# Performance work log

Measured on AMD Instinct MI355X. Metric: run time of the kernel, lower is better.

## Reference

```python
import jax, jax.numpy as jnp
import numpy as np

B, S, D = 2, 2048, 4096
NH, NKV, HD = 32, 8, 128
NREP = NH // NKV
ROPE_THETA = 10000.0


def setup_inputs() -> dict:
    key = jax.random.key(0)
    k1, k2, k3, k4, k5 = jax.random.split(key, 5)
    x = jax.random.normal(k1, (B, S, D), jnp.float32)
    wq = jax.random.normal(k2, (NH * HD, D), jnp.float32) * 0.02
    wk = jax.random.normal(k3, (NKV * HD, D), jnp.float32) * 0.02
    wv = jax.random.normal(k4, (NKV * HD, D), jnp.float32) * 0.02
    wo = jax.random.normal(k5, (D, NH * HD), jnp.float32) * 0.02
    inv_freq = 1.0 / (ROPE_THETA ** (np.arange(0, HD, 2, dtype=np.float64) / HD))
    ang = np.outer(np.arange(S, dtype=np.float64), inv_freq)  # [S, HD/2]
    return {
        'x': x, 'start_pos': 0,
        'freqs_cos': jnp.asarray(np.cos(ang), jnp.float32),
        'freqs_sin': jnp.asarray(np.sin(ang), jnp.float32),
        'wq': wq, 'wk': wk, 'wv': wv, 'wo': wo,
    }


def _apply_rope(x, cos, sin):
    # x: [B, S, H, HD]; cos/sin: [S, HD/2]. Matches torch view_as_complex on
    # interleaved (even, odd) feature pairs: (xr + i*xi) * (cos + i*sin).
    xr = x[..., 0::2]
    xi = x[..., 1::2]
    c = cos[None, :, None, :]
    s = sin[None, :, None, :]
    out_r = xr * c - xi * s
    out_i = xr * s + xi * c
    return jnp.stack([out_r, out_i], axis=-1).reshape(x.shape)


def reference(x, start_pos, freqs_cos, freqs_sin, wq, wk, wv, wo):
    b, s, _ = x.shape
    xq = (x @ wq.T).reshape(b, s, NH, HD)
    xk = (x @ wk.T).reshape(b, s, NKV, HD)
    xv = (x @ wv.T).reshape(b, s, NKV, HD)
    # Source applies RoPE to K and V (not Q) -- reproduced faithfully.
    xk = _apply_rope(xk, freqs_cos, freqs_sin)
    xv = _apply_rope(xv, freqs_cos, freqs_sin)
    # start_pos == 0 prefill: cache slice [:, :start_pos+s] == freshly written xk/xv.
    # repeat_kv: head h_out = h_kv * NREP + rep  ==  jnp.repeat along head axis.
    keys = jnp.repeat(xk, NREP, axis=2)    # [B, S, NH, HD]
    values = jnp.repeat(xv, NREP, axis=2)  # [B, S, NH, HD]
    scale = 1.0 / jnp.sqrt(jnp.asarray(HD, x.dtype))
    scores = jnp.einsum('bqhd,bkhd->bhqk', xq, keys) * scale  # [B, NH, S, S]
    probs = jax.nn.softmax(scores, axis=-1)  # NOTE: no causal mask in source
    out = jnp.einsum('bhqk,bkhd->bqhd', probs, values).reshape(b, s, NH * HD)
    return out @ wo.T
```

## Files before the change

### kernel.cpp

```cpp
#include <hip/hip_runtime.h>
#include <hip/hip_bf16.h>


typedef short bf16x8 __attribute__((ext_vector_type(8)));
typedef float f32x4 __attribute__((ext_vector_type(4)));

__device__ __forceinline__ void load16(const void* g, void* l) {
  __builtin_amdgcn_global_load_lds(
      (const __attribute__((address_space(1))) void*)g,
      (__attribute__((address_space(3))) void*)l, 16, 0, 0);
}

__device__ __forceinline__ f32x4 mfma16(bf16x8 a, bf16x8 b, f32x4 c) {
  return __builtin_amdgcn_mfma_f32_16x16x32_bf16(a, b, c, 0, 0, 0);
}

__device__ __forceinline__ unsigned short f2b(float f) {
  union { float f; unsigned int u; } v; v.f = f;
  unsigned int u = v.u;
  return (unsigned short)((u + 0x7fffu + ((u >> 16) & 1u)) >> 16);
}
__device__ __forceinline__ float b2f(unsigned short u) {
  union { unsigned int u; float f; } v; v.u = ((unsigned int)u) << 16;
  return v.f;
}
__device__ __forceinline__ unsigned short f2b_fast(float f) {
  __hip_bfloat16 h = __float2bfloat16(f);
  return *reinterpret_cast<unsigned short*>(&h);
}

#define QSCALE (0.08838834764831845f * 1.4426950408889634f)

__global__ __launch_bounds__(256) void cvt_f32_bf16(
    const float* __restrict__ in, unsigned short* __restrict__ out, int n4) {
  int idx = blockIdx.x * 256 + threadIdx.x;
  int stride = gridDim.x * 256;
  for (int i = idx; i < n4; i += stride) {
    float4 v = reinterpret_cast<const float4*>(in)[i];
    ushort4 o;
    o.x = f2b(v.x); o.y = f2b(v.y); o.z = f2b(v.z); o.w = f2b(v.w);
    reinterpret_cast<ushort4*>(out)[i] = o;
  }
}

template <typename OutT>
__global__ __launch_bounds__(512, 2) void gemm256(
    const unsigned short* __restrict__ A, const unsigned short* __restrict__ Bw,
    OutT* __restrict__ C, int M, int N, int K, int sbl) {
  extern __shared__ char smem[];
  const int tid = threadIdx.x;
  const int lane = tid & 63;
  const int w = tid >> 6;
  const int lr = lane & 15, lg = lane >> 4;
  const int wr = w >> 2, wc = w & 3;

  const int nbn = N >> 8;
  const int bid = blockIdx.x, nwg = gridDim.x;
  const int swz = (bid & 7) * (nwg >> 3) + (bid >> 3);
  const int bm = swz / nbn, bn = swz % nbn;

  const unsigned short* Ag = A + (size_t)bm * 256 * K;
  const unsigned short* Bg = Bw + (size_t)bn * 256 * K;

  int aoffs[4], boffs[4], sdst[4];
#pragma unroll
  for (int j = 0; j < 4; ++j) {
    const int c = tid + j * 512;
    const int u = c >> 3;
    const int slot = ((c & 7) ^ (u & 7)) << 3;
    aoffs[j] = u * K + slot;
    const int br = ((u & 127) >> 5) * 64 + (u >> 7) * 32 + (u & 31);
    boffs[j] = br * K + slot;
    sdst[j] = ((tid & ~63) << 4) + j * 8192;
  }

#define ST_A(hh, tt)                                                          \
  {                                                                           \
    char* d = smem + (((tt)&1) * 65536);                                      \
    load16(Ag + aoffs[(hh)] + ((tt) << 6), d + sdst[(hh)]);                   \
    load16(Ag + aoffs[(hh) + 2] + ((tt) << 6), d + sdst[(hh) + 2]);           \
  }
#define ST_B(hh, tt)                                                          \
  {                                                                           \
    char* d = smem + (((tt)&1) * 65536) + 32768;                              \
    load16(Bg + boffs[(hh)*2] + ((tt) << 6), d + sdst[(hh)*2]);               \
    load16(Bg + boffs[(hh)*2 + 1] + ((tt) << 6), d + sdst[(hh)*2 + 1]);       \
  }
#define GATE10                                                                \
  asm volatile("s_waitcnt vmcnt(10)" ::: "memory");                           \
  __builtin_amdgcn_s_barrier();
#define LGKM0                                                                 \
  asm volatile("s_waitcnt lgkmcnt(0)" ::: "memory");                          \
  __builtin_amdgcn_sched_barrier(0);

  f32x4 acc[8][4];
#pragma unroll
  for (int m = 0; m < 8; ++m)
#pragma unroll
    for (int n = 0; n < 4; ++n) acc[m][n] = (f32x4){0.f, 0.f, 0.f, 0.f};

  ST_A(0, 0); ST_B(0, 0); ST_B(1, 0); ST_A(1, 0);
  ST_A(0, 1); ST_B(0, 1); ST_B(1, 1);

  const int NT = K >> 6;
  const int NI = NT >> 1;
  const int xr = (lr & 7) << 4;
  const int aBase = (wr * 128 + lr) * 128;
  const int bBase = (wc * 32 + lr) * 128;
  const int col0 = (lg * 16) ^ xr;
  const int col1 = (64 + lg * 16) ^ xr;

  bf16x8 aR[4][2], b01[2][2], b23[2][2];

  for (int i = 0; i < NI; ++i) {
    const int T1 = 2 * i + 1;
    const int te = (2 * i + 2 < NT) ? 2 * i + 2 : 0;
    const int to = (2 * i + 3 < NT) ? 2 * i + 3 : 1;
    const char* d0 = smem;
    const char* d1 = smem + 65536;

    GATE10;
#pragma unroll
    for (int mf = 0; mf < 4; ++mf) {
      aR[mf][0] = *(const bf16x8*)(d0 + aBase + mf * 2048 + col0);
      aR[mf][1] = *(const bf16x8*)(d0 + aBase + mf * 2048 + col1);
    }
#pragma unroll
    for (int nf = 0; nf < 2; ++nf) {
      b01[nf][0] = *(const bf16x8*)(d0 + 32768 + bBase + nf * 2048 + col0);
      b01[nf][1] = *(const bf16x8*)(d0 + 32768 + bBase + nf * 2048 + col1);
    }
    ST_A(1, T1);
    LGKM0;
    __builtin_amdgcn_s_setprio(1);
#pragma unroll
    for (int mf = 0; mf < 4; ++mf)
#pragma unroll
      for (int nf = 0; nf < 2; ++nf) {
        acc[mf][nf] = mfma16(aR[mf][0], b01[nf][0], acc[mf][nf]);
        acc[mf][nf] = mfma16(aR[mf][1], b01[nf][1], acc[mf][nf]);
      }
    __builtin_amdgcn_s_setprio(0);

    GATE10;
#pragma unroll
    for (int nf = 0; nf < 2; ++nf) {
      b23[nf][0] = *(const bf16x8*)(d0 + 32768 + 16384 + bBase + nf * 2048 + col0);
      b23[nf][1] = *(const bf16x8*)(d0 + 32768 + 16384 + bBase + nf * 2048 + col1);
    }
    ST_A(0, te);
    LGKM0;
    __builtin_amdgcn_s_setprio(1);
#pragma unroll
    for (int mf = 0; mf < 4; ++mf)
#pragma unroll
      for (int nf = 0; nf < 2; ++nf) {
        acc[mf][2 + nf] = mfma16(aR[mf][0], b23[nf][0], acc[mf][2 + nf]);
        acc[mf][2 + nf] = mfma16(aR[mf][1], b23[nf][1], acc[mf][2 + nf]);
      }
    __builtin_amdgcn_s_setprio(0);

    GATE10;
#pragma unroll
    for (int mf = 0; mf < 4; ++mf) {
      aR[mf][0] = *(const bf16x8*)(d0 + aBase + (4 + mf) * 2048 + col0);
      aR[mf][1] = *(const bf16x8*)(d0 + aBase + (4 + mf) * 2048 + col1);
    }
    ST_B(0, te);
    LGKM0;
    __builtin_amdgcn_s_setprio(1);
#pragma unroll
    for (int mf = 0; mf < 4; ++mf)
#pragma unroll
      for (int nf = 0; nf < 2; ++nf) {
        acc[4 + mf][nf] = mfma16(aR[mf][0], b01[nf][0], acc[4 + mf][nf]);
        acc[4 + mf][nf] = mfma16(aR[mf][1], b01[nf][1], acc[4 + mf][nf]);
      }
    __builtin_amdgcn_s_setprio(0);

    ST_B(1, te);
    __builtin_amdgcn_s_setprio(1);
#pragma unroll
    for (int mf = 0; mf < 4; ++mf)
#pragma unroll
      for (int nf = 0; nf < 2; ++nf) {
        acc[4 + mf][2 + nf] = mfma16(aR[mf][0], b23[nf][0], acc[4 + mf][2 + nf]);
        acc[4 + mf][2 + nf] = mfma16(aR[mf][1], b23[nf][1], acc[4 + mf][2 + nf]);
      }
    __builtin_amdgcn_s_setprio(0);

    GATE10;
#pragma unroll
    for (int mf = 0; mf < 4; ++mf) {
      aR[mf][0] = *(const bf16x8*)(d1 + aBase + mf * 2048 + col0);
      aR[mf][1] = *(const bf16x8*)(d1 + aBase + mf * 2048 + col1);
    }
#pragma unroll
    for (int nf = 0; nf < 2; ++nf) {
      b01[nf][0] = *(const bf16x8*)(d1 + 32768 + bBase + nf * 2048 + col0);
      b01[nf][1] = *(const bf16x8*)(d1 + 32768 + bBase + nf * 2048 + col1);
    }
    ST_A(1, te);
    LGKM0;
    __builtin_amdgcn_s_setprio(1);
#pragma unroll
    for (int mf = 0; mf < 4; ++mf)
#pragma unroll
      for (int nf = 0; nf < 2; ++nf) {
        acc[mf][nf] = mfma16(aR[mf][0], b01[nf][0], acc[mf][nf]);
        acc[mf][nf] = mfma16(aR[mf][1], b01[nf][1], acc[mf][nf]);
      }
    __builtin_amdgcn_s_setprio(0);

    GATE10;
#pragma unroll
    for (int nf = 0; nf < 2; ++nf) {
      b23[nf][0] = *(const bf16x8*)(d1 + 32768 + 16384 + bBase + nf * 2048 + col0);
      b23[nf][1] = *(const bf16x8*)(d1 + 32768 + 16384 + bBase + nf * 2048 + col1);
    }
    ST_A(0, to);
    LGKM0;
    __builtin_amdgcn_s_setprio(1);
#pragma unroll
    for (int mf = 0; mf < 4; ++mf)
#pragma unroll
      for (int nf = 0; nf < 2; ++nf) {
        acc[mf][2 + nf] = mfma16(aR[mf][0], b23[nf][0], acc[mf][2 + nf]);
        acc[mf][2 + nf] = mfma16(aR[mf][1], b23[nf][1], acc[mf][2 + nf]);
      }
    __builtin_amdgcn_s_setprio(0);

    GATE10;
#pragma unroll
    for (int mf = 0; mf < 4; ++mf) {
      aR[mf][0] = *(const bf16x8*)(d1 + aBase + (4 + mf) * 2048 + col0);
      aR[mf][1] = *(const bf16x8*)(d1 + aBase + (4 + mf) * 2048 + col1);
    }
    ST_B(0, to);
    LGKM0;
    __builtin_amdgcn_s_setprio(1);
#pragma unroll
    for (int mf = 0; mf < 4; ++mf)
#pragma unroll
      for (int nf = 0; nf < 2; ++nf) {
        acc[4 + mf][nf] = mfma16(aR[mf][0], b01[nf][0], acc[4 + mf][nf]);
        acc[4 + mf][nf] = mfma16(aR[mf][1], b01[nf][1], acc[4 + mf][nf]);
      }
    __builtin_amdgcn_s_setprio(0);

    ST_B(1, to);
    __builtin_amdgcn_s_setprio(1);
#pragma unroll
    for (int mf = 0; mf < 4; ++mf)
#pragma unroll
      for (int nf = 0; nf < 2; ++nf) {
        acc[4 + mf][2 + nf] = mfma16(aR[mf][0], b23[nf][0], acc[4 + mf][2 + nf]);
        acc[4 + mf][2 + nf] = mfma16(aR[mf][1], b23[nf][1], acc[4 + mf][2 + nf]);
      }
    __builtin_amdgcn_s_setprio(0);
  }
#undef ST_A
#undef ST_B
#undef GATE10
#undef LGKM0

  const float cscale = (bn < sbl) ? QSCALE : 1.0f;
#pragma unroll
  for (int mf = 0; mf < 8; ++mf)
#pragma unroll
    for (int nf = 0; nf < 4; ++nf)
#pragma unroll
      for (int r = 0; r < 4; ++r) {
        int rowc = bm * 256 + wr * 128 + mf * 16 + lg * 4 + r;
        int colc = bn * 256 + wc * 64 + nf * 16 + lr;
        float v = acc[mf][nf][r] * cscale;
        if constexpr (sizeof(OutT) == 2)
          C[(size_t)rowc * N + colc] = (OutT)f2b(v);
        else
          C[(size_t)rowc * N + colc] = v;
      }
}

__global__ __launch_bounds__(256) void rope_kv(
    const unsigned short* __restrict__ XQKV,
    const float* __restrict__ fc, const float* __restrict__ fs,
    unsigned short* __restrict__ Kr, unsigned short* __restrict__ Vt) {
  __shared__ unsigned short Vl[128][66];
  const int t = threadIdx.x;
  const int bid = blockIdx.x;
  const int stile = bid & 31, bkv = bid >> 5;
  const int b = bkv >> 3, kvh = bkv & 7;
  const int s0 = stile * 64;
  const int l = t & 63;
  const int jrow = t >> 6;

  for (int j = 0; j < 16; ++j) {
    int s = s0 + j * 4 + jrow;
    ushort2 v = *(const ushort2*)(XQKV + (size_t)(b * 2048 + s) * 6144 + 4096 +
                                  kvh * 128 + 2 * l);
    float c = fc[s * 64 + l], sn = fs[s * 64 + l];
    float xr = b2f(v.x), xi = b2f(v.y);
    ushort2 o;
    o.x = f2b(xr * c - xi * sn);
    o.y = f2b(xr * sn + xi * c);
    *(ushort2*)(Kr + ((size_t)bkv * 2048 + s) * 128 + 2 * l) = o;
  }
  for (int j = 0; j < 16; ++j) {
    int ss = j * 4 + jrow;
    int s = s0 + ss;
    ushort2 v = *(const ushort2*)(XQKV + (size_t)(b * 2048 + s) * 6144 + 5120 +
                                  kvh * 128 + 2 * l);
    float c = fc[s * 64 + l], sn = fs[s * 64 + l];
    float xr = b2f(v.x), xi = b2f(v.y);
    Vl[2 * l][ss] = f2b(xr * c - xi * sn);
    Vl[2 * l + 1][ss] = f2b(xr * sn + xi * c);
  }
  __syncthreads();
  const int d = t >> 1, half = t & 1;
  unsigned short* vdst = Vt + ((size_t)bkv * 128 + d) * 2048 + s0 + half * 32;
#pragma unroll
  for (int e = 0; e < 32; e += 4) {
    ushort4 pk;
    pk.x = Vl[d][half * 32 + e];
    pk.y = Vl[d][half * 32 + e + 1];
    pk.z = Vl[d][half * 32 + e + 2];
    pk.w = Vl[d][half * 32 + e + 3];
    *(ushort4*)(vdst + e) = pk;
  }
}

__global__ __launch_bounds__(256, 2) void attn_fwd(
    const unsigned short* __restrict__ XQ, const unsigned short* __restrict__ Kr,
    const unsigned short* __restrict__ Vt, unsigned short* __restrict__ AO) {
  extern __shared__ char smem[];
  char* Ksm = smem;
  char* Vsm = smem + 16384;
  unsigned short* Ps = (unsigned short*)(smem + 32768);
  const int t = threadIdx.x;
  const int lane = t & 63, w = t >> 6;
  const int lr = lane & 15, lg = lane >> 4;

  const int bid = blockIdx.x;
  const int nwg = gridDim.x;
  const int swz = (bid & 7) * (nwg >> 3) + (bid >> 3);
  const int qt = swz & 7;
  const int bh = swz >> 3;
  const int b = bh >> 5, h = bh & 31;
  const int bkv = b * 8 + (h >> 2);

  bf16x8 qf[4][4];
#pragma unroll
  for (int q4 = 0; q4 < 4; ++q4) {
    const unsigned short* qp =
        XQ + ((size_t)(b * 2048 + qt * 256 + w * 64 + q4 * 16 + lr)) * 6144 +
        h * 128 + lg * 8;
#pragma unroll
    for (int dc = 0; dc < 4; ++dc) qf[q4][dc] = *(const bf16x8*)(qp + dc * 32);
  }

  f32x4 acc[4][8];
#pragma unroll
  for (int q4 = 0; q4 < 4; ++q4)
#pragma unroll
    for (int i = 0; i < 8; ++i) acc[q4][i] = (f32x4){0.f, 0.f, 0.f, 0.f};
  float l_[4][4];
#pragma unroll
  for (int q4 = 0; q4 < 4; ++q4)
#pragma unroll
    for (int r = 0; r < 4; ++r) l_[q4][r] = 0.f;

  const unsigned short* Kbase = Kr + (size_t)bkv * 2048 * 128;
  const unsigned short* Vbase = Vt + (size_t)bkv * 128 * 2048;

  const int c0 = t, c1 = t + 256;
  const int kK0 = c0 & 31, dC0 = c0 >> 5;
  const int kK1 = c1 & 31, dC1 = c1 >> 5;
  const int vD0 = c0 & 127, vKc0 = c0 >> 7;
  const int vD1 = c1 & 127, vKc1 = c1 >> 7;
  const int dstb0 = (c0 & ~63) * 16;
  const int dstb1 = (c1 & ~63) * 16;

#define STAGE_KV(bufi, kt)                                                     \
  {                                                                            \
    char* kd = Ksm + (bufi)*8192;                                              \
    char* vd = Vsm + (bufi)*8192;                                              \
    load16(Kbase + (size_t)((kt)*32 + kK0) * 128 + dC0 * 8, kd + dstb0);       \
    load16(Kbase + (size_t)((kt)*32 + kK1) * 128 + dC1 * 8, kd + dstb1);       \
    load16(Vbase + (size_t)vD0 * 2048 + (kt)*32 + vKc0 * 8, vd + dstb0);       \
    load16(Vbase + (size_t)vD1 * 2048 + (kt)*32 + vKc1 * 8, vd + dstb1);       \
  }

  STAGE_KV(0, 0);
  asm volatile("s_waitcnt vmcnt(0)" ::: "memory");
  __builtin_amdgcn_s_barrier();

  unsigned short* Pw = Ps + w * 2048;
  const int pbase = (lr >> 3) * 512 + (lr & 7);

  for (int kt = 0; kt < 64; ++kt) {
    const int cur = kt & 1;
    if (kt < 63) STAGE_KV(cur ^ 1, kt + 1);

    const char* Kc = Ksm + cur * 8192;
    const char* Vc = Vsm + cur * 8192;

#pragma unroll
    for (int nf = 0; nf < 2; ++nf) {
      f32x4 s[4];
#pragma unroll
      for (int q4 = 0; q4 < 4; ++q4) s[q4] = (f32x4){0.f, 0.f, 0.f, 0.f};
#pragma unroll
      for (int dc = 0; dc < 4; ++dc) {
        bf16x8 kf =
            *(const bf16x8*)(Kc + ((dc * 4 + lg) * 32 + nf * 16 + lr) * 16);
#pragma unroll
        for (int q4 = 0; q4 < 4; ++q4) s[q4] = mfma16(qf[q4][dc], kf, s[q4]);
      }
      const int pb = pbase + nf * 1024;
#pragma unroll
      for (int q4 = 0; q4 < 4; ++q4)
#pragma unroll
        for (int r = 0; r < 4; ++r) {
          float p = __builtin_amdgcn_exp2f(s[q4][r]);
          l_[q4][r] += p;
          Pw[pb + (q4 * 16 + lg * 4 + r) * 8] = f2b_fast(p);
        }
    }

    bf16x8 pf[4];
#pragma unroll
    for (int q4 = 0; q4 < 4; ++q4)
      pf[q4] = *(const bf16x8*)(Pw + lg * 512 + (q4 * 16 + lr) * 8);
#pragma unroll
    for (int dt = 0; dt < 8; ++dt) {
      bf16x8 vf = *(const bf16x8*)(Vc + (lg * 128 + dt * 16 + lr) * 16);
#pragma unroll
      for (int q4 = 0; q4 < 4; ++q4)
        acc[q4][dt] = mfma16(pf[q4], vf, acc[q4][dt]);
    }

    asm volatile("s_waitcnt vmcnt(0)" ::: "memory");
    __builtin_amdgcn_s_barrier();
  }
#undef STAGE_KV

#pragma unroll
  for (int q4 = 0; q4 < 4; ++q4)
#pragma unroll
    for (int r = 0; r < 4; ++r) {
#pragma unroll
      for (int o = 1; o < 16; o <<= 1) l_[q4][r] += __shfl_xor(l_[q4][r], o);
    }

#pragma unroll
  for (int q4 = 0; q4 < 4; ++q4)
#pragma unroll
    for (int r = 0; r < 4; ++r) {
      float inv = 1.f / l_[q4][r];
      size_t rowb =
          ((size_t)(b * 2048 + qt * 256 + w * 64 + q4 * 16 + lg * 4 + r)) * 4096 +
          h * 128;
#pragma unroll
      for (int dt = 0; dt < 8; ++dt)
        AO[rowb + dt * 16 + lr] = f2b_fast(acc[q4][dt][r] * inv);
    }
}

extern "C" void kernel_launch(void* const* d_in, const int* in_sizes, int n_in,
                              void* d_out, int out_size, void* d_ws, size_t ws_size,
                              hipStream_t stream) {
  const float* x  = (const float*)d_in[0];
  const float* fc = (const float*)d_in[2];
  const float* fs = (const float*)d_in[3];
  const float* wq = (const float*)d_in[4];
  const float* wk = (const float*)d_in[5];
  const float* wv = (const float*)d_in[6];
  const float* wo = (const float*)d_in[7];

  const size_t MB = 1024ull * 1024ull;
  char* ws = (char*)d_ws;
  unsigned short* Xb   = (unsigned short*)(ws);
  unsigned short* Wsc  = (unsigned short*)(ws + 32 * MB);
  unsigned short* Kr   = (unsigned short*)(ws);
  unsigned short* Vt   = (unsigned short*)(ws + 8 * MB);
  unsigned short* AO   = (unsigned short*)(ws + 80 * MB);
  unsigned short* XQKV = (unsigned short*)d_out;

  (void)hipFuncSetAttribute((const void*)gemm256<unsigned short>,
                            hipFuncAttributeMaxDynamicSharedMemorySize, 131072);
  (void)hipFuncSetAttribute((const void*)gemm256<float>,
                            hipFuncAttributeMaxDynamicSharedMemorySize, 131072);
  (void)hipFuncSetAttribute((const void*)attn_fwd,
                            hipFuncAttributeMaxDynamicSharedMemorySize, 49152);

  dim3 blk(256);
  dim3 blk512(512);
  cvt_f32_bf16<<<2048, blk, 0, stream>>>(x, Xb, (2 * 2048 * 4096) / 4);
  cvt_f32_bf16<<<2048, blk, 0, stream>>>(wq, Wsc, (4096 * 4096) / 4);
  cvt_f32_bf16<<<2048, blk, 0, stream>>>(wk, Wsc + 4096 * 4096, (1024 * 4096) / 4);
  cvt_f32_bf16<<<2048, blk, 0, stream>>>(wv, Wsc + 5120 * 4096, (1024 * 4096) / 4);
  gemm256<unsigned short><<<384, blk512, 131072, stream>>>(
      Xb, Wsc, XQKV, 4096, 6144, 4096, 16);
  rope_kv<<<512, blk, 0, stream>>>(XQKV, fc, fs, Kr, Vt);
  attn_fwd<<<512, blk, 49152, stream>>>(XQKV, Kr, Vt, AO);
  cvt_f32_bf16<<<2048, blk, 0, stream>>>(wo, Wsc, (4096 * 4096) / 4);
  gemm256<float><<<256, blk512, 131072, stream>>>(
      AO, Wsc, (float*)d_out, 4096, 4096, 4096, 0);
}
```

Measured before the change: 542.9 us.

## Use BK=32 double-buffered GEMM for QKV projection and merge weight conversions

Adds a variant of the 256x256 bf16 MFMA GEMM with a 32-wide K tile and 64KB of LDS, double-buffered across two stages with interleaved global-to-LDS loads and MFMA phases. It is used for the fused QKV projection, and the three weight-conversion launches are merged into one kernel. The smaller LDS footprint and finer pipelining aim to improve latency hiding, at the cost of more barriers per unit of K.

```diff
diff --git a/kernel.cpp b/kernel.cpp
--- a/kernel.cpp
+++ b/kernel.cpp
@@ -41,6 +41,228 @@
     o.x = f2b(v.x); o.y = f2b(v.y); o.z = f2b(v.z); o.w = f2b(v.w);
     reinterpret_cast<ushort4*>(out)[i] = o;
   }
+}
+
+__global__ __launch_bounds__(256) void cvt_w3(
+    const float* __restrict__ wq, const float* __restrict__ wk,
+    const float* __restrict__ wv, unsigned short* __restrict__ out) {
+  const int nq = 4096 * 4096 / 4, nk = 1024 * 4096 / 4;
+  const int tot = nq + 2 * nk;
+  int idx = blockIdx.x * 256 + threadIdx.x;
+  int stride = gridDim.x * 256;
+  for (int i = idx; i < tot; i += stride) {
+    int j = i;
+    const float4* src;
+    if (j < nq) {
+      src = reinterpret_cast<const float4*>(wq);
+    } else if (j < nq + nk) {
+      src = reinterpret_cast<const float4*>(wk); j -= nq;
+    } else {
+      src = reinterpret_cast<const float4*>(wv); j -= nq + nk;
+    }
+    float4 v = src[j];
+    ushort4 o;
+    o.x = f2b(v.x); o.y = f2b(v.y); o.z = f2b(v.z); o.w = f2b(v.w);
+    reinterpret_cast<ushort4*>(out)[i] = o;
+  }
+}
+
+template <typename OutT>
+__global__ __launch_bounds__(512, 2) void gemm256_bk32(
+    const unsigned short* __restrict__ A, const unsigned short* __restrict__ Bw,
+    OutT* __restrict__ C, int M, int N, int K, int sbl) {
+  extern __shared__ char smem[];
+  const int tid = threadIdx.x;
+  const int lane = tid & 63;
+  const int w = tid >> 6;
+  const int lr = lane & 15, lg = lane >> 4;
+  const int wr = w >> 2, wc = w & 3;
+
+  const int nbn = N >> 8;
+  const int bid = blockIdx.x, nwg = gridDim.x;
+  const int swz = (bid & 7) * (nwg >> 3) + (bid >> 3);
+  const int bm = swz / nbn, bn = swz % nbn;
+
+  const unsigned short* Ag = A + (size_t)bm * 256 * K;
+  const unsigned short* Bg = Bw + (size_t)bn * 256 * K;
+
+  const int arow = tid & 255;
+  const int akc = tid >> 8;
+  const int sd0 = (tid & ~63) * 16;
+
+#define ST_A0(tt) load16(Ag + (size_t)arow * K + (tt)*32 + akc * 8,           \
+                         smem + ((tt)&1) * 32768 + sd0)
+#define ST_A1(tt) load16(Ag + (size_t)arow * K + (tt)*32 + (akc + 2) * 8,     \
+                         smem + ((tt)&1) * 32768 + sd0 + 8192)
+#define ST_B0(tt) load16(Bg + (size_t)arow * K + (tt)*32 + akc * 8,           \
+                         smem + ((tt)&1) * 32768 + 16384 + sd0)
+#define ST_B1(tt) load16(Bg + (size_t)arow * K + (tt)*32 + (akc + 2) * 8,     \
+                         smem + ((tt)&1) * 32768 + 16384 + sd0 + 8192)
+#define BAR __builtin_amdgcn_s_barrier()
+#define GATE2                                                                 \
+  asm volatile("s_waitcnt vmcnt(2)" ::: "memory");                            \
+  __builtin_amdgcn_s_barrier();
+#define LGKM0                                                                 \
+  asm volatile("s_waitcnt lgkmcnt(0)" ::: "memory");                          \
+  __builtin_amdgcn_sched_barrier(0);
+
+  f32x4 acc[8][4];
+#pragma unroll
+  for (int m = 0; m < 8; ++m)
+#pragma unroll
+    for (int n = 0; n < 4; ++n) acc[m][n] = (f32x4){0.f, 0.f, 0.f, 0.f};
+
+  ST_B0(0); ST_A0(0); ST_A1(0); ST_B1(0); ST_B0(1); ST_A0(1);
+
+  const int NT = K >> 5;
+  const int NI = NT >> 1;
+  const int aRowB = (wr * 128 + lr) * 16;
+  const int bRowB = (wc * 64 + lr) * 16;
+
+  bf16x8 aR[4], b01[2], b23[2];
+
+  for (int i = 0; i < NI; ++i) {
+    const int T1 = 2 * i + 1;
+    const int te = (2 * i + 2 < NT) ? 2 * i + 2 : 0;
+    const int to = (2 * i + 3 < NT) ? 2 * i + 3 : 1;
+    const char* d0A = smem;
+    const char* d0B = smem + 16384;
+    const char* d1A = smem + 32768;
+    const char* d1B = smem + 49152;
+
+    GATE2;
+#pragma unroll
+    for (int mf = 0; mf < 4; ++mf)
+      aR[mf] = *(const bf16x8*)(d0A + lg * 4096 + aRowB + mf * 256);
+#pragma unroll
+    for (int nf = 0; nf < 2; ++nf)
+      b01[nf] = *(const bf16x8*)(d0B + lg * 4096 + bRowB + nf * 256);
+    ST_A1(T1);
+    LGKM0;
+    __builtin_amdgcn_s_setprio(1);
+#pragma unroll
+    for (int mf = 0; mf < 4; ++mf)
+#pragma unroll
+      for (int nf = 0; nf < 2; ++nf)
+        acc[mf][nf] = mfma16(aR[mf], b01[nf], acc[mf][nf]);
+    __builtin_amdgcn_s_setprio(0);
+
+    BAR;
+#pragma unroll
+    for (int nf = 0; nf < 2; ++nf)
+      b23[nf] = *(const bf16x8*)(d0B + lg * 4096 + bRowB + (2 + nf) * 256);
+    ST_B1(T1);
+    LGKM0;
+    __builtin_amdgcn_s_setprio(1);
+#pragma unroll
+    for (int mf = 0; mf < 4; ++mf)
+#pragma unroll
+      for (int nf = 0; nf < 2; ++nf)
+        acc[mf][2 + nf] = mfma16(aR[mf], b23[nf], acc[mf][2 + nf]);
+    __builtin_amdgcn_s_setprio(0);
+
+    BAR;
+#pragma unroll
+    for (int mf = 0; mf < 4; ++mf)
+      aR[mf] = *(const bf16x8*)(d0A + lg * 4096 + aRowB + (4 + mf) * 256);
+    ST_B0(te);
+    LGKM0;
+    __builtin_amdgcn_s_setprio(1);
+#pragma unroll
+    for (int mf = 0; mf < 4; ++mf)
+#pragma unroll
+      for (int nf = 0; nf < 2; ++nf)
+        acc[4 + mf][nf] = mfma16(aR[mf], b01[nf], acc[4 + mf][nf]);
+    __builtin_amdgcn_s_setprio(0);
+
+    BAR;
+    ST_A0(te);
+    __builtin_amdgcn_s_setprio(1);
+#pragma unroll
+    for (int mf = 0; mf < 4; ++mf)
+#pragma unroll
+      for (int nf = 0; nf < 2; ++nf)
+        acc[4 + mf][2 + nf] = mfma16(aR[mf], b23[nf], acc[4 + mf][2 + nf]);
+    __builtin_amdgcn_s_setprio(0);
+
+    GATE2;
+#pragma unroll
+    for (int mf = 0; mf < 4; ++mf)
+      aR[mf] = *(const bf16x8*)(d1A + lg * 4096 + aRowB + mf * 256);
+#pragma unroll
+    for (int nf = 0; nf < 2; ++nf)
+      b01[nf] = *(const bf16x8*)(d1B + lg * 4096 + bRowB + nf * 256);
+    ST_A1(te);
+    LGKM0;
+    __builtin_amdgcn_s_setprio(1);
+#pragma unroll
+    for (int mf = 0; mf < 4; ++mf)
+#pragma unroll
+      for (int nf = 0; nf < 2; ++nf)
+        acc[mf][nf] = mfma16(aR[mf], b01[nf], acc[mf][nf]);
+    __builtin_amdgcn_s_setprio(0);
+
+    BAR;
+#pragma unroll
+    for (int nf = 0; nf < 2; ++nf)
+      b23[nf] = *(const bf16x8*)(d1B + lg * 4096 + bRowB + (2 + nf) * 256);
+    ST_B1(te);
+    LGKM0;
+    __builtin_amdgcn_s_setprio(1);
+#pragma unroll
+    for (int mf = 0; mf < 4; ++mf)
+#pragma unroll
+      for (int nf = 0; nf < 2; ++nf)
+        acc[mf][2 + nf] = mfma16(aR[mf], b23[nf], acc[mf][2 + nf]);
+    __builtin_amdgcn_s_setprio(0);
+
+    BAR;
+#pragma unroll
+    for (int mf = 0; mf < 4; ++mf)
+      aR[mf] = *(const bf16x8*)(d1A + lg * 4096 + aRowB + (4 + mf) * 256);
+    ST_B0(to);
+    LGKM0;
+    __builtin_amdgcn_s_setprio(1);
+#pragma unroll
+    for (int mf = 0; mf < 4; ++mf)
+#pragma unroll
+      for (int nf = 0; nf < 2; ++nf)
+        acc[4 + mf][nf] = mfma16(aR[mf], b01[nf], acc[4 + mf][nf]);
+    __builtin_amdgcn_s_setprio(0);
+
+    BAR;
+    ST_A0(to);
+    __builtin_amdgcn_s_setprio(1);
+#pragma unroll
+    for (int mf = 0; mf < 4; ++mf)
+#pragma unroll
+      for (int nf = 0; nf < 2; ++nf)
+        acc[4 + mf][2 + nf] = mfma16(aR[mf], b23[nf], acc[4 + mf][2 + nf]);
+    __builtin_amdgcn_s_setprio(0);
+  }
+#undef ST_A0
+#undef ST_A1
+#undef ST_B0
+#undef ST_B1
+#undef BAR
+#undef GATE2
+#undef LGKM0
+
+  const float cscale = (bn < sbl) ? QSCALE : 1.0f;
+#pragma unroll
+  for (int mf = 0; mf < 8; ++mf)
+#pragma unroll
+    for (int nf = 0; nf < 4; ++nf)
+#pragma unroll
+      for (int r = 0; r < 4; ++r) {
+        int rowc = bm * 256 + wr * 128 + mf * 16 + lg * 4 + r;
+        int colc = bn * 256 + wc * 64 + nf * 16 + lr;
+        float v = acc[mf][nf][r] * cscale;
+        if constexpr (sizeof(OutT) == 2)
+          C[(size_t)rowc * N + colc] = (OutT)f2b(v);
+        else
+          C[(size_t)rowc * N + colc] = v;
+      }
 }
 
 template <typename OutT>
@@ -486,8 +708,8 @@
   unsigned short* AO   = (unsigned short*)(ws + 80 * MB);
   unsigned short* XQKV = (unsigned short*)d_out;
 
-  (void)hipFuncSetAttribute((const void*)gemm256<unsigned short>,
-                            hipFuncAttributeMaxDynamicSharedMemorySize, 131072);
+  (void)hipFuncSetAttribute((const void*)gemm256_bk32<unsigned short>,
+                            hipFuncAttributeMaxDynamicSharedMemorySize, 65536);
   (void)hipFuncSetAttribute((const void*)gemm256<float>,
                             hipFuncAttributeMaxDynamicSharedMemorySize, 131072);
   (void)hipFuncSetAttribute((const void*)attn_fwd,
@@ -496,10 +718,8 @@
   dim3 blk(256);
   dim3 blk512(512);
   cvt_f32_bf16<<<2048, blk, 0, stream>>>(x, Xb, (2 * 2048 * 4096) / 4);
-  cvt_f32_bf16<<<2048, blk, 0, stream>>>(wq, Wsc, (4096 * 4096) / 4);
-  cvt_f32_bf16<<<2048, blk, 0, stream>>>(wk, Wsc + 4096 * 4096, (1024 * 4096) / 4);
-  cvt_f32_bf16<<<2048, blk, 0, stream>>>(wv, Wsc + 5120 * 4096, (1024 * 4096) / 4);
-  gemm256<unsigned short><<<384, blk512, 131072, stream>>>(
+  cvt_w3<<<2048, blk, 0, stream>>>(wq, wk, wv, Wsc);
+  gemm256_bk32<unsigned short><<<384, blk512, 65536, stream>>>(
       Xb, Wsc, XQKV, 4096, 6144, 4096, 16);
   rope_kv<<<512, blk, 0, stream>>>(XQKV, fc, fs, Kr, Vt);
   attn_fwd<<<512, blk, 49152, stream>>>(XQKV, Kr, Vt, AO);
```

Measured after the change: 674.5 us. 1.24x slower.
